# Kernel tuning notes

Hardware: AMD Instinct MI355X
Metric: run time of the kernel (lower is better)

Reference implementation:

```python
import jax, jax.numpy as jnp
import numpy as np

IN_FEATURES = 4096
OUT_FEATURES = 4096
MAX_RANK = 32
ALPHA = 32
SCALING = ALPHA / MAX_RANK  # 1.0


def setup_inputs() -> dict:
    key = jax.random.key(0)
    k_x, k_u, k_v = jax.random.split(key, 3)
    x = jax.random.normal(k_x, (4, 2048, IN_FEATURES), dtype=jnp.float32)
    U = jax.random.normal(k_u, (OUT_FEATURES, MAX_RANK), dtype=jnp.float32) * 0.01
    S = jnp.ones((MAX_RANK,), dtype=jnp.float32)
    V = jax.random.normal(k_v, (MAX_RANK, IN_FEATURES), dtype=jnp.float32) * 0.01
    return {"x": x, "U": U, "S": S, "V": V}


def reference(x, U, S, V):
    # Original: W = U @ diag(S) @ V ; out = (x @ W.T) * scaling  (dropout=0 -> Identity)
    # Mathematically identical factored form: ((x @ V^T) * S) @ U^T * scaling.
    h = jnp.einsum('bsi,ri->bsr', x, V)        # [B,S,rank]
    h = h * S                                   # scale by singular values
    out = jnp.einsum('bsr,or->bso', h, U)       # [B,S,out]
    return out * SCALING
```

## Files before the change

kernel.cpp:

```cpp
#include <hip/hip_runtime.h>
#include <hip/hip_bf16.h>

typedef __bf16 bf16x8 __attribute__((ext_vector_type(8)));
typedef float  f32x4  __attribute__((ext_vector_type(4)));

#define IN_F   4096
#define OUT_F  4096
#define RANK   32

__device__ __forceinline__ bf16x8 cvt8(float4 a, float4 b) {
    bf16x8 r;
    r[0] = (__bf16)a.x; r[1] = (__bf16)a.y; r[2] = (__bf16)a.z; r[3] = (__bf16)a.w;
    r[4] = (__bf16)b.x; r[5] = (__bf16)b.y; r[6] = (__bf16)b.z; r[7] = (__bf16)b.w;
    return r;
}

__device__ __forceinline__ void gl_lds16(const float* g, void* l) {
    __builtin_amdgcn_global_load_lds(
        (const __attribute__((address_space(1))) char*)g,
        (__attribute__((address_space(3))) char*)l, 16, 0, 0);
}

template <int KS>
__global__ __launch_bounds__(256, 2)
void lora_h(const float* __restrict__ X, const float* __restrict__ S,
            const float* __restrict__ V, float* __restrict__ Hpart)
{
    constexpr int F    = IN_F / KS;
    constexpr int NCHK = F / 64;

    __shared__ float4 XB[2][4][2][2][64];
    __shared__ float4 VB[2][2][2][2][64];
    __shared__ float  Hp[4][64][17];

    const int tid  = threadIdx.x;
    const int wave = tid >> 6;
    const int lane = tid & 63;
    const int r    = lane & 15;
    const int kg   = lane >> 4;

    const int rh = wave & 1;
    const int fs = wave >> 1;

    const int t0    = blockIdx.x * 64;
    const int fbase = blockIdx.y * F;

    auto stage = [&](int c, int nb) {
        const int fc = fbase + ((c + blockIdx.x) & (NCHK - 1)) * 64;
        #pragma unroll
        for (int t = 0; t < 6; ++t) {
            const int inst = wave * 6 + t;
            if (inst < 16) {
                const int tt = inst >> 2, s = (inst >> 1) & 1, h2 = inst & 1;
                gl_lds16(X + (size_t)(t0 + tt * 16 + r) * IN_F
                           + fc + s * 32 + h2 * 16 + kg * 4,
                         (void*)&XB[nb][tt][s][h2][0]);
            } else {
                const int v = inst - 16;
                const int vr = v >> 2, s = (v >> 1) & 1, h2 = v & 1;
                gl_lds16(V + (size_t)(vr * 16 + r) * IN_F
                           + fc + s * 32 + h2 * 16 + kg * 4,
                         (void*)&VB[nb][vr][s][h2][0]);
            }
        }
    };

    const int h  = kg >> 1;
    const int qb = (kg & 1) * 2;

    f32x4 acc[4] = {};

    auto compute = [&](int cur) {
        float4 v0 = *(const float4*)&VB[cur][rh][fs][h][qb * 16 + r];
        float4 v1 = *(const float4*)&VB[cur][rh][fs][h][(qb + 1) * 16 + r];
        bf16x8 vb = cvt8(v0, v1);
        #pragma unroll
        for (int tt = 0; tt < 4; ++tt) {
            float4 x0 = *(const float4*)&XB[cur][tt][fs][h][qb * 16 + r];
            float4 x1 = *(const float4*)&XB[cur][tt][fs][h][(qb + 1) * 16 + r];
            acc[tt] = __builtin_amdgcn_mfma_f32_16x16x32_bf16(
                          cvt8(x0, x1), vb, acc[tt], 0, 0, 0);
        }
    };

    stage(0, 0);
    for (int c = 0; c < NCHK; ++c) {
        const int cur = c & 1;
        if (c + 1 < NCHK) {
            stage(c + 1, cur ^ 1);
            asm volatile("s_waitcnt vmcnt(6)" ::: "memory");
        } else {
            asm volatile("s_waitcnt vmcnt(0)" ::: "memory");
        }
        __builtin_amdgcn_s_barrier();
        __builtin_amdgcn_sched_barrier(0);
        compute(cur);
        __builtin_amdgcn_s_barrier();
    }

    #pragma unroll
    for (int tt = 0; tt < 4; ++tt)
        #pragma unroll
        for (int j = 0; j < 4; ++j)
            Hp[wave][tt * 16 + kg * 4 + j][r] = acc[tt][j];
    __syncthreads();

    float* dst = Hpart + ((size_t)blockIdx.y * 8192 + t0) * RANK;
    for (int i = tid; i < 64 * RANK; i += 256) {
        const int tok = i >> 5, rr = i & 31;
        const int rhh = rr >> 4, ri = rr & 15;
        const float s = Hp[rhh][tok][ri] + Hp[2 + rhh][tok][ri];
        dst[i] = s * S[rr];
    }
}

template <int NKS>
__global__ __launch_bounds__(256, 4)
void lora_out(const float* __restrict__ Hpart, const float* __restrict__ U,
              float* __restrict__ Out)
{
    __shared__ float Hs[128][33];

    const int tid  = threadIdx.x;
    const int wave = tid >> 6;
    const int lane = tid & 63;
    const int r    = lane & 15;
    const int kg   = lane >> 4;

    const int tt = blockIdx.x >> 6;
    const int cq = blockIdx.x & 63;
    const int t0 = tt * 128;
    const int c0 = cq * 64;

    float4 ua[4][2];
    #pragma unroll
    for (int b = 0; b < 4; ++b) {
        const float4* up = reinterpret_cast<const float4*>(
            U + (size_t)(c0 + b * 16 + r) * RANK + kg * 8);
        ua[b][0] = up[0];
        ua[b][1] = up[1];
    }

    #pragma unroll
    for (int k4 = 0; k4 < 4; ++k4) {
        const int fidx = tid + k4 * 256;
        float4 v = {0.f, 0.f, 0.f, 0.f};
        #pragma unroll
        for (int k = 0; k < NKS; ++k) {
            const float4* hp = reinterpret_cast<const float4*>(
                Hpart + ((size_t)k * 8192 + t0) * RANK);
            float4 p = hp[fidx];
            v.x += p.x; v.y += p.y; v.z += p.z; v.w += p.w;
        }
        const int tok = fidx >> 3;
        const int rr  = (fidx & 7) * 4;
        Hs[tok][rr] = v.x; Hs[tok][rr + 1] = v.y;
        Hs[tok][rr + 2] = v.z; Hs[tok][rr + 3] = v.w;
    }
    __syncthreads();

    bf16x8 ub[4];
    #pragma unroll
    for (int b = 0; b < 4; ++b) ub[b] = cvt8(ua[b][0], ua[b][1]);

    #pragma unroll
    for (int ai = 0; ai < 2; ++ai) {
        const int a = wave + ai * 4;
        bf16x8 hb;
        #pragma unroll
        for (int j = 0; j < 8; ++j) hb[j] = (__bf16)Hs[a * 16 + r][kg * 8 + j];
        float* orow = Out + (size_t)(t0 + a * 16 + r) * OUT_F + c0 + kg * 4;
        #pragma unroll
        for (int b = 0; b < 4; ++b) {
            f32x4 d = {0.f, 0.f, 0.f, 0.f};
            d = __builtin_amdgcn_mfma_f32_16x16x32_bf16(ub[b], hb, d, 0, 0, 0);
            *reinterpret_cast<float4*>(orow + b * 16) = *reinterpret_cast<float4*>(&d);
        }
    }
}

extern "C" void kernel_launch(void* const* d_in, const int* in_sizes, int n_in,
                              void* d_out, int out_size, void* d_ws, size_t ws_size,
                              hipStream_t stream) {
    const float* X = (const float*)d_in[0];
    const float* U = (const float*)d_in[1];
    const float* S = (const float*)d_in[2];
    const float* V = (const float*)d_in[3];
    float* Out   = (float*)d_out;
    float* Hpart = (float*)d_ws;

    if (ws_size >= (size_t)4 * 1024 * 1024) {
        lora_h<4><<<dim3(128, 4), 256, 0, stream>>>(X, S, V, Hpart);
        lora_out<4><<<4096, 256, 0, stream>>>(Hpart, U, Out);
    } else {
        lora_h<1><<<dim3(128, 1), 256, 0, stream>>>(X, S, V, Hpart);
        lora_out<1><<<4096, 256, 0, stream>>>(Hpart, U, Out);
    }
}
```

Measured before the change: 70.73 us.

## Triple-buffer H kernel, split K-reduction into separate kernel, per-wave token tiles

The rank-projection kernel moves from double to triple buffering of the X/V chunks in LDS, so two chunks are in flight while one is computed. Each wave now owns a 16-token tile over the full 64-wide K slice. This removes the cross-wave LDS reduction and the Hp scratch array, and results are written straight to global with S applied. A new small kernel sums the K-split partials into H once, so the output kernel no longer reads four partials per block. The cost is an extra kernel launch, more LDS per block (which may lower occupancy), and a larger workspace requirement.

```diff
diff --git a/kernel.cpp b/kernel.cpp
--- a/kernel.cpp
+++ b/kernel.cpp
@@ -29,9 +29,8 @@
     constexpr int F    = IN_F / KS;
     constexpr int NCHK = F / 64;
 
-    __shared__ float4 XB[2][4][2][2][64];
-    __shared__ float4 VB[2][2][2][2][64];
-    __shared__ float  Hp[4][64][17];
+    __shared__ float4 XB[3][4][2][2][64];
+    __shared__ float4 VB[3][2][2][2][64];
 
     const int tid  = threadIdx.x;
     const int wave = tid >> 6;
@@ -39,11 +38,11 @@
     const int r    = lane & 15;
     const int kg   = lane >> 4;
 
-    const int rh = wave & 1;
-    const int fs = wave >> 1;
-
     const int t0    = blockIdx.x * 64;
     const int fbase = blockIdx.y * F;
+
+    const float s_lo = S[r];
+    const float s_hi = S[16 + r];
 
     auto stage = [&](int c, int nb) {
         const int fc = fbase + ((c + blockIdx.x) & (NCHK - 1)) * 64;
@@ -68,55 +67,68 @@
     const int h  = kg >> 1;
     const int qb = (kg & 1) * 2;
 
-    f32x4 acc[4] = {};
+    f32x4 acc[2] = {};
 
     auto compute = [&](int cur) {
-        float4 v0 = *(const float4*)&VB[cur][rh][fs][h][qb * 16 + r];
-        float4 v1 = *(const float4*)&VB[cur][rh][fs][h][(qb + 1) * 16 + r];
-        bf16x8 vb = cvt8(v0, v1);
-        #pragma unroll
-        for (int tt = 0; tt < 4; ++tt) {
-            float4 x0 = *(const float4*)&XB[cur][tt][fs][h][qb * 16 + r];
-            float4 x1 = *(const float4*)&XB[cur][tt][fs][h][(qb + 1) * 16 + r];
-            acc[tt] = __builtin_amdgcn_mfma_f32_16x16x32_bf16(
-                          cvt8(x0, x1), vb, acc[tt], 0, 0, 0);
+        #pragma unroll
+        for (int s = 0; s < 2; ++s) {
+            float4 x0 = *(const float4*)&XB[cur][wave][s][h][qb * 16 + r];
+            float4 x1 = *(const float4*)&XB[cur][wave][s][h][(qb + 1) * 16 + r];
+            bf16x8 xb = cvt8(x0, x1);
+            #pragma unroll
+            for (int rh = 0; rh < 2; ++rh) {
+                float4 v0 = *(const float4*)&VB[cur][rh][s][h][qb * 16 + r];
+                float4 v1 = *(const float4*)&VB[cur][rh][s][h][(qb + 1) * 16 + r];
+                acc[rh] = __builtin_amdgcn_mfma_f32_16x16x32_bf16(
+                              xb, cvt8(v0, v1), acc[rh], 0, 0, 0);
+            }
         }
     };
 
     stage(0, 0);
+    stage(1, 1);
+
     for (int c = 0; c < NCHK; ++c) {
-        const int cur = c & 1;
-        if (c + 1 < NCHK) {
-            stage(c + 1, cur ^ 1);
+        if (c + 2 < NCHK) {
+            stage(c + 2, (c + 2) % 3);
+            asm volatile("s_waitcnt vmcnt(12)" ::: "memory");
+        } else if (c + 1 < NCHK) {
             asm volatile("s_waitcnt vmcnt(6)" ::: "memory");
         } else {
             asm volatile("s_waitcnt vmcnt(0)" ::: "memory");
         }
         __builtin_amdgcn_s_barrier();
         __builtin_amdgcn_sched_barrier(0);
-        compute(cur);
+        compute(c % 3);
         __builtin_amdgcn_s_barrier();
     }
 
-    #pragma unroll
-    for (int tt = 0; tt < 4; ++tt)
-        #pragma unroll
-        for (int j = 0; j < 4; ++j)
-            Hp[wave][tt * 16 + kg * 4 + j][r] = acc[tt][j];
-    __syncthreads();
-
-    float* dst = Hpart + ((size_t)blockIdx.y * 8192 + t0) * RANK;
-    for (int i = tid; i < 64 * RANK; i += 256) {
-        const int tok = i >> 5, rr = i & 31;
-        const int rhh = rr >> 4, ri = rr & 15;
-        const float s = Hp[rhh][tok][ri] + Hp[2 + rhh][tok][ri];
-        dst[i] = s * S[rr];
+    float* Hq = Hpart + ((size_t)blockIdx.y * 8192 + t0) * RANK;
+    #pragma unroll
+    for (int j = 0; j < 4; ++j) {
+        const int tok = wave * 16 + kg * 4 + j;
+        Hq[(size_t)tok * RANK + r]      = acc[0][j] * s_lo;
+        Hq[(size_t)tok * RANK + 16 + r] = acc[1][j] * s_hi;
     }
 }
 
 template <int NKS>
+__global__ __launch_bounds__(256)
+void lora_hred(const float* __restrict__ Hpart, float* __restrict__ H)
+{
+    const int idx = blockIdx.x * 256 + threadIdx.x;
+    const float4* hp = reinterpret_cast<const float4*>(Hpart);
+    float4 v = hp[idx];
+    #pragma unroll
+    for (int k = 1; k < NKS; ++k) {
+        float4 p = hp[(size_t)k * 65536 + idx];
+        v.x += p.x; v.y += p.y; v.z += p.z; v.w += p.w;
+    }
+    reinterpret_cast<float4*>(H)[idx] = v;
+}
+
 __global__ __launch_bounds__(256, 4)
-void lora_out(const float* __restrict__ Hpart, const float* __restrict__ U,
+void lora_out(const float* __restrict__ H, const float* __restrict__ U,
               float* __restrict__ Out)
 {
     __shared__ float Hs[128][33];
@@ -141,17 +153,11 @@
         ua[b][1] = up[1];
     }
 
+    const float4* hsrc = reinterpret_cast<const float4*>(H + (size_t)t0 * RANK);
     #pragma unroll
     for (int k4 = 0; k4 < 4; ++k4) {
         const int fidx = tid + k4 * 256;
-        float4 v = {0.f, 0.f, 0.f, 0.f};
-        #pragma unroll
-        for (int k = 0; k < NKS; ++k) {
-            const float4* hp = reinterpret_cast<const float4*>(
-                Hpart + ((size_t)k * 8192 + t0) * RANK);
-            float4 p = hp[fidx];
-            v.x += p.x; v.y += p.y; v.z += p.z; v.w += p.w;
-        }
+        float4 v = hsrc[fidx];
         const int tok = fidx >> 3;
         const int rr  = (fidx & 7) * 4;
         Hs[tok][rr] = v.x; Hs[tok][rr + 1] = v.y;
@@ -186,14 +192,17 @@
     const float* U = (const float*)d_in[1];
     const float* S = (const float*)d_in[2];
     const float* V = (const float*)d_in[3];
-    float* Out   = (float*)d_out;
-    float* Hpart = (float*)d_ws;
-
-    if (ws_size >= (size_t)4 * 1024 * 1024) {
+    float* Out = (float*)d_out;
+
+    float* H     = (float*)d_ws;
+    float* Hpart = (float*)d_ws + 262144;
+
+    if (ws_size >= (size_t)5 * 1024 * 1024) {
         lora_h<4><<<dim3(128, 4), 256, 0, stream>>>(X, S, V, Hpart);
-        lora_out<4><<<4096, 256, 0, stream>>>(Hpart, U, Out);
+        lora_hred<4><<<256, 256, 0, stream>>>(Hpart, H);
+        lora_out<<<4096, 256, 0, stream>>>(H, U, Out);
     } else {
-        lora_h<1><<<dim3(128, 1), 256, 0, stream>>>(X, S, V, Hpart);
-        lora_out<1><<<4096, 256, 0, stream>>>(Hpart, U, Out);
-    }
-}
+        lora_h<1><<<dim3(128, 1), 256, 0, stream>>>(X, S, V, H);
+        lora_out<<<4096, 256, 0, stream>>>(H, U, Out);
+    }
+}
```

Measured after the change: 68.32 us. 1.04x faster.
